# Kernel optimization log

Hardware: AMD Instinct MI355X
Metric: run time of the kernel (lower is better)

The kernel has to match this reference:

```python
import jax, jax.numpy as jnp
from jax import lax
import numpy as np

SIGMA = 25.0
NUM_STEPS = 100
DT = 0.01
SQRT_DT = float(np.sqrt(DT))


def _score(x, eig, t, cond, W1, we, wt, b1, Wc, W2, b2):
    # x: [B,S,H], eig: [B,S], t: scalar, cond: [B,S,H] or None
    h = x @ W1 + eig[..., None] * we + t * wt + b1
    if cond is not None:
        h = h + cond @ Wc
    h = jax.nn.silu(h)
    return h @ W2 + b2


def _diffuse(x_T, eigvals, eigvecs, cond, params, key):
    # reverse SDE from t=1 to t=0 in NUM_STEPS steps
    ts = jnp.linspace(1.0, 0.0, NUM_STEPS)
    keys = jax.random.split(key, NUM_STEPS)
    VT = jnp.swapaxes(eigvecs, -2, -1)  # [B,S,S]

    def step(x, tk):
        t, k = tk
        x_spec = VT @ x                                   # spectral projection [B,S,H]
        score = _score(x_spec, eigvals, t, cond, *params)
        drift = -(SIGMA ** (2.0 * t)) * score
        noise = jax.random.normal(k, x.shape, x.dtype)
        x_new = x - drift * DT + (SIGMA ** t) * SQRT_DT * noise
        return x_new, None

    x, _ = lax.scan(step, x_T, (ts, keys))
    return x


def _make_net(key, H, scale):
    k = jax.random.split(key, 4)
    return dict(
        W1=jax.random.normal(k[0], (H, H), jnp.float32) * scale,
        we=jax.random.normal(k[1], (H,), jnp.float32) * scale,
        wt=jax.random.normal(k[2], (H,), jnp.float32) * scale,
        b1=jnp.zeros((H,), jnp.float32),
        Wc=jax.random.normal(k[3], (H, H), jnp.float32) * scale,
        W2=jax.random.normal(jax.random.fold_in(key, 99), (H, H), jnp.float32) * scale,
        b2=jnp.zeros((H,), jnp.float32),
    )


def setup_inputs() -> dict:
    key = jax.random.key(0)
    B, S, H = 4, 512, 256
    ks = jax.random.split(key, 9)
    inp = {}
    inp['features_text'] = jax.random.normal(ks[0], (B, S, H), jnp.float32)
    inp['features_audio'] = jax.random.normal(ks[1], (B, S, H), jnp.float32)
    inp['features_visual'] = jax.random.normal(ks[2], (B, S, H), jnp.float32)
    sg = jax.random.normal(ks[3], (B, S, S), jnp.float32)
    inp['speaker_graph'] = 0.5 * (sg + jnp.swapaxes(sg, -2, -1))  # symmetric for eigh
    tg = jax.random.normal(ks[4], (B, S, S), jnp.float32)
    inp['temporal_graph'] = 0.5 * (tg + jnp.swapaxes(tg, -2, -1))
    # only text modality (index 0) is missing -> diffusion path for text only
    inp['missing_mask'] = jnp.zeros((B, S, 3), bool).at[:, :, 0].set(True)
    inp['x_T'] = jax.random.normal(ks[5], (B, S, H), jnp.float32)
    scale = 1.0 / np.sqrt(H)
    for prefix, k in [('ts', ks[6]), ('tt', ks[7])]:  # text_speaker / text_temporal nets
        net = _make_net(k, H, scale)
        for name, v in net.items():
            inp[f'{prefix}_{name}'] = v
    kr = jax.random.split(ks[8], 2)
    inp['rec_W'] = jax.random.normal(kr[0], (H, H), jnp.float32) * scale
    inp['rec_b'] = jnp.zeros((H,), jnp.float32)
    return inp


def reference(features_text, features_audio, features_visual,
              speaker_graph, temporal_graph, missing_mask, x_T,
              ts_W1, ts_we, ts_wt, ts_b1, ts_Wc, ts_W2, ts_b2,
              tt_W1, tt_we, tt_wt, tt_b1, tt_Wc, tt_W2, tt_b2,
              rec_W, rec_b):
    # spectral decomposition of both graphs
    s_vals, s_vecs = jnp.linalg.eigh(speaker_graph)
    t_vals, t_vecs = jnp.linalg.eigh(temporal_graph)

    feats = {'text': features_text, 'audio': features_audio, 'visual': features_visual}
    miss = np.asarray(missing_mask)  # concrete branching as in torch forward
    any_missing = [bool(miss[:, :, i].any()) for i in range(3)]

    params = {'text': (
        (ts_W1, ts_we, ts_wt, ts_b1, ts_Wc, ts_W2, ts_b2),
        (tt_W1, tt_we, tt_wt, tt_b1, tt_Wc, tt_W2, tt_b2))}
    key = jax.random.key(42)

    recovered = {}
    for i, modality in enumerate(['text', 'audio', 'visual']):
        if any_missing[i]:
            # condition = mean of present (non-missing) other modalities
            cond_feats = [feats[m] for j, m in enumerate(['text', 'audio', 'visual'])
                          if m != modality and not any_missing[j]]
            cond = None
            if cond_feats:
                cond = jnp.mean(jnp.stack(cond_feats, axis=-1), axis=-1)
            k_s, k_t = jax.random.split(jax.random.fold_in(key, i))
            p_s, p_t = params[modality]
            x_s = _diffuse(x_T, s_vals, s_vecs, cond, p_s, k_s)
            x_t = _diffuse(x_T, t_vals, t_vecs, cond, p_t, k_t)
            rec = 0.5 * (x_s + x_t)
            recovered[modality] = rec @ rec_W + rec_b
        else:
            recovered[modality] = feats[modality]
    return (recovered['text'], recovered['audio'], recovered['visual'])
```

## Files before the change

kernel.cpp:

```cpp
#include <hip/hip_runtime.h>
#include <math.h>
#include <stdint.h>


#define NT 256
#define SZF 131072
#define MATSZ 262144
#define NB 32
#define ILAST 384
#define TBASE (ILAST+1)
#define TSZ (512-TBASE)

#define BD_DK   0
#define BD_ZK   4096
#define BD_RZK  8192
#define BD_TAU  12288
#define BD_DS   16384
#define BD_RHO  20480
#define BD_KSK  20736
#define BD_KIDX 22784
#define BD_DIDX 24832
#define BD_PERM 26880
#define BD_CNT  28928

#define ALD(p)    __hip_atomic_load((p),  __ATOMIC_RELAXED, __HIP_MEMORY_SCOPE_AGENT)
#define AST(p,v)  __hip_atomic_store((p), (v), __ATOMIC_RELAXED, __HIP_MEMORY_SCOPE_AGENT)

__host__ __device__ static inline unsigned rotl32(unsigned v, int r){ return (v<<r)|(v>>(32-r)); }

__host__ __device__ static inline void tf2x32(unsigned k0, unsigned k1,
                                              unsigned x0, unsigned x1,
                                              unsigned* o0, unsigned* o1){
  unsigned ks2 = k0 ^ k1 ^ 0x1BD11BDAu;
  x0 += k0; x1 += k1;
#define TF4(r0,r1,r2,r3) \
  x0 += x1; x1 = rotl32(x1,r0); x1 ^= x0; \
  x0 += x1; x1 = rotl32(x1,r1); x1 ^= x0; \
  x0 += x1; x1 = rotl32(x1,r2); x1 ^= x0; \
  x0 += x1; x1 = rotl32(x1,r3); x1 ^= x0;
  TF4(13,15,26,6)  x0 += k1;  x1 += ks2 + 1u;
  TF4(17,29,16,24) x0 += ks2; x1 += k0 + 2u;
  TF4(13,15,26,6)  x0 += k0;  x1 += k1 + 3u;
  TF4(17,29,16,24) x0 += k1;  x1 += ks2 + 4u;
  TF4(13,15,26,6)  x0 += ks2; x1 += k0 + 5u;
#undef TF4
  *o0 = x0; *o1 = x1;
}

__device__ static inline float erfinv_xla(float x){
  float w = -log1pf(-x*x);
  float p;
  if (w < 5.0f){
    w -= 2.5f;
    p = 2.81022636e-08f;
    p = fmaf(p, w, 3.43273939e-07f);
    p = fmaf(p, w, -3.5233877e-06f);
    p = fmaf(p, w, -4.39150654e-06f);
    p = fmaf(p, w, 0.00021858087f);
    p = fmaf(p, w, -0.00125372503f);
    p = fmaf(p, w, -0.00417768164f);
    p = fmaf(p, w, 0.246640727f);
    p = fmaf(p, w, 1.50140941f);
  } else {
    w = sqrtf(w) - 3.0f;
    p = -0.000200214257f;
    p = fmaf(p, w, 0.000100950558f);
    p = fmaf(p, w, 0.00134934322f);
    p = fmaf(p, w, -0.00367342844f);
    p = fmaf(p, w, 0.00573950773f);
    p = fmaf(p, w, -0.0076224613f);
    p = fmaf(p, w, 0.00943887047f);
    p = fmaf(p, w, 1.00167406f);
    p = fmaf(p, w, 2.83297682f);
  }
  return p*x;
}

__device__ static inline float bits_to_normal(unsigned bits){
  const float MINV = -0.99999994f;
  float f = __uint_as_float((bits >> 9) | 0x3f800000u) - 1.0f;
  float u = fmaxf(MINV, fmaf(f, 2.0f, MINV));
  return 1.41421356237309515f * erfinv_xla(u);
}

__device__ __forceinline__ void gbar2(unsigned* slots, int sg, int g, unsigned epoch){
  __threadfence_block();
  __syncthreads();
  int t = threadIdx.x;
  if (t == 0) AST(slots + (sg*NB + g)*16, epoch);
  if (t < NB){
    unsigned* sl = slots + (sg*NB + t)*16;
    while (ALD(sl) < epoch){ __builtin_amdgcn_s_sleep(1); }
  }
  __syncthreads();
}

__global__ __launch_bounds__(256) void k_sytd2_lds(const float* Gs, const float* Gt,
                                                   double* Vb, double* smalls,
                                                   unsigned* slots, double* Atail){
  int sg = blockIdx.x / NB, g = blockIdx.x % NB;
  const float* G = (sg < 4) ? (Gs + (size_t)sg*MATSZ) : (Gt + (size_t)(sg-4)*MATSZ);
  double* V = Vb + (size_t)sg*MATSZ;
  double* d  = smalls + (size_t)sg*512;
  double* e  = smalls + 4096 + (size_t)sg*512;
  double* tu = smalls + 8192 + (size_t)sg*512;
  double* acc0 = smalls + 274688 + (size_t)sg*512;
  double* acc1 = acc0 + 4096;
  double* col0 = smalls + 282880 + (size_t)sg*512;
  double* col1 = col0 + 4096;
  double* vvh  = smalls + 291072 + (size_t)sg*512;
  double* At = Atail + (size_t)sg*MATSZ;
  int t = threadIdx.x, wave = t >> 6, lane = t & 63;

  __shared__ double Arows[16][512];
  __shared__ double vv[512], wv[512], col2[512], acc[512];
  __shared__ double red[4];
  __shared__ double bc[4];

  for (int j=0; j<16; j++){
    int r = 32*j + g;
    for (int c=t; c<512; c+=256)
      Arows[j][c] = (double)G[(size_t)r*512 + c];
  }

  for (int r=t; r<512; r+=256) col2[r] = (r>=1) ? (double)G[(size_t)r*512] : 0.0;
  __syncthreads();
  {
    double part = 0.0;
    for (int r=2+t; r<512; r+=256) part += col2[r]*col2[r];
    #pragma unroll
    for (int off=32; off; off>>=1) part += __shfl_down(part, off, 64);
    if (lane==0) red[wave]=part;
    __syncthreads();
    if (t==0){
      double xsq = red[0]+red[1]+red[2]+red[3];
      double alpha = col2[1];
      double beta,tv,scal;
      if (xsq == 0.0){ beta=alpha; tv=0.0; scal=0.0; }
      else {
        beta = -copysign(sqrt(alpha*alpha + xsq), alpha);
        tv = (beta - alpha)/beta;
        scal = 1.0/(alpha - beta);
      }
      if (g==0){ e[0]=beta; tu[0]=tv; }
      bc[0]=tv; bc[1]=scal;
    }
  }
  __syncthreads();
  double tauv = bc[0];
  {
    double scal = bc[1];
    for (int r=t; r<512; r+=256){
      double v = 0.0;
      if (r==1) v = 1.0;
      else if (r>1) v = (tauv==0.0) ? 0.0 : col2[r]*scal;
      vv[r]=v;
      if (r>=1 && (r & (NB-1))==g) V[r] = v;
    }
  }
  __syncthreads();
  if (g==0){
    for (int r=1+t; r<512; r+=256) AST(&col0[r], (double)G[(size_t)r*512 + 1]);
  }
  {
    int r0 = 1 + ((g - 1) & (NB-1));
    for (int r = r0 + NB*wave; r < 512; r += 4*NB){
      const double* Ar = Arows[r>>5];
      double p = 0.0;
      for (int c=lane; c<512; c+=64) p += Ar[c]*vv[c];
      #pragma unroll
      for (int off=32; off; off>>=1) p += __shfl_down(p, off, 64);
      if (lane==0) AST(&acc0[r], p);
    }
  }

  for (int i=0; i<ILAST; i++){
    gbar2(slots, sg, g, (unsigned)(i+1));
    int lo=i+1, lo2=i+2;
    double* accR = (i&1) ? acc1 : acc0;
    double* colR = (i&1) ? col1 : col0;
    double* accW = (i&1) ? acc0 : acc1;
    double* colW = (i&1) ? col0 : col1;
    double part = 0.0;
    for (int r=lo+t; r<512; r+=256){
      double a_ = ALD(&accR[r]);
      double c_ = ALD(&colR[r]);
      acc[r]=a_; col2[r]=c_;
      part += (tauv*a_)*vv[r];
    }
    #pragma unroll
    for (int off=32; off; off>>=1) part += __shfl_down(part, off, 64);
    if (lane==0) red[wave]=part;
    __syncthreads();
    {
      double dot = red[0]+red[1]+red[2]+red[3];
      double alpha2 = -0.5*tauv*dot;
      double vlo = vv[lo];
      double wlo = fma(alpha2, vlo, tauv*acc[lo]);
      for (int r=lo+t; r<512; r+=256){
        double wr = fma(alpha2, vv[r], tauv*acc[r]);
        wv[r]=wr;
        col2[r] = col2[r] - vv[r]*wlo - wr*vlo;
      }
    }
    __syncthreads();
    part = 0.0;
    for (int r=lo2+1+t; r<512; r+=256) part += col2[r]*col2[r];
    #pragma unroll
    for (int off=32; off; off>>=1) part += __shfl_down(part, off, 64);
    if (lane==0) red[wave]=part;
    __syncthreads();
    double tau2, scal2;
    {
      double xsq = red[0]+red[1]+red[2]+red[3];
      double alpha = col2[lo2];
      double beta;
      if (xsq == 0.0){ beta=alpha; tau2=0.0; scal2=0.0; }
      else {
        beta = -copysign(sqrt(alpha*alpha + xsq), alpha);
        tau2 = (beta - alpha)/beta;
        scal2 = 1.0/(alpha - beta);
      }
      if (t==0 && g==0){ e[lo]=beta; tu[lo]=tau2; }
    }
    {
      double vvc[8], wvc[8], v2c[8];
      #pragma unroll
      for (int j=0;j<8;j++){
        int c = lo + lane + 64*j;
        bool ok = c < 512;
        vvc[j] = ok ? vv[c] : 0.0;
        wvc[j] = ok ? wv[c] : 0.0;
        double v2v = 0.0;
        if (ok){
          if (c==lo2) v2v = 1.0;
          else if (c>lo2) v2v = (tau2==0.0) ? 0.0 : col2[c]*scal2;
        }
        v2c[j] = v2v;
      }
      int r0 = lo + ((g - lo) & (NB-1));
      for (int r = r0 + NB*wave; r < 512; r += 4*NB){
        double* Ar = Arows[r>>5];
        double vr = vv[r], wr = wv[r];
        double p = 0.0;
        #pragma unroll
        for (int j=0;j<8;j++){
          int c = lo + lane + 64*j;
          if (c < 512){
            double an = Ar[c] - vr*wvc[j] - wr*vvc[j];
            Ar[c] = an;
            p += an * v2c[j];
            if (c == lo2) AST(&colW[r], an);
          }
        }
        #pragma unroll
        for (int off=32; off; off>>=1) p += __shfl_down(p, off, 64);
        if (lane==0) AST(&accW[r], p);
      }
    }
    __syncthreads();
    for (int r=t; r<512; r+=256){
      double v = 0.0;
      if (r==lo2) v = 1.0;
      else if (r>lo2) v = (tau2==0.0) ? 0.0 : col2[r]*scal2;
      vv[r]=v;
      if (r>=lo2 && (r & (NB-1))==g) V[(size_t)lo*512 + r] = v;
    }
    tauv = tau2;
  }

  if (t < 16){
    int r = 32*t + g;
    if (r <= ILAST) d[r] = Arows[t][r];
  }
  for (int j=0; j<16; j++){
    int r = 32*j + g;
    if (r >= TBASE){
      for (int c=TBASE+t; c<512; c+=256)
        At[(size_t)r*512 + c] = Arows[j][c];
    }
  }
  if (g==0){
    for (int r=t; r<512; r+=256) vvh[r] = vv[r];
  }
}

__global__ __launch_bounds__(256) void k_sy_tail(const double* Atail, double* Vb,
                                                 double* smalls){
  int sg = blockIdx.x;
  double* V = Vb + (size_t)sg*MATSZ;
  double* d  = smalls + (size_t)sg*512;
  double* e  = smalls + 4096 + (size_t)sg*512;
  double* tu = smalls + 8192 + (size_t)sg*512;
  const double* accG = smalls + 274688 + (size_t)sg*512;
  const double* colG = smalls + 282880 + (size_t)sg*512;
  const double* vvG  = smalls + 291072 + (size_t)sg*512;
  const double* At0 = Atail + (size_t)sg*MATSZ;
  int t = threadIdx.x, wave = t >> 6, lane = t & 63;

  __shared__ double At[TSZ*128];
  __shared__ double vv[512], wv[512], col2[512], acc[512], accN[512], colN[512];
  __shared__ double red[4];

  for (int rl=0; rl<TSZ; rl++)
    for (int cl=t; cl<TSZ; cl+=256)
      At[rl*128+cl] = At0[(size_t)(TBASE+rl)*512 + TBASE+cl];
  for (int r=t; r<512; r+=256){
    if (r >= ILAST){ vv[r]=vvG[r]; acc[r]=accG[r]; col2[r]=colG[r]; }
  }
  double tauv = tu[ILAST];
  __syncthreads();

  for (int i=ILAST; i<510; i++){
    int lo=i+1, lo2=i+2;
    double part = 0.0;
    for (int r=lo+t; r<512; r+=256) part += (tauv*acc[r])*vv[r];
    #pragma unroll
    for (int off=32; off; off>>=1) part += __shfl_down(part, off, 64);
    if (lane==0) red[wave]=part;
    __syncthreads();
    {
      double dot = red[0]+red[1]+red[2]+red[3];
      double alpha2 = -0.5*tauv*dot;
      double vlo = vv[lo];
      double wlo = fma(alpha2, vlo, tauv*acc[lo]);
      for (int r=lo+t; r<512; r+=256){
        double wr = fma(alpha2, vv[r], tauv*acc[r]);
        wv[r]=wr;
        col2[r] = col2[r] - vv[r]*wlo - wr*vlo;
      }
    }
    __syncthreads();
    part = 0.0;
    for (int r=lo2+1+t; r<512; r+=256) part += col2[r]*col2[r];
    #pragma unroll
    for (int off=32; off; off>>=1) part += __shfl_down(part, off, 64);
    if (lane==0) red[wave]=part;
    __syncthreads();
    double tau2, scal2;
    {
      double xsq = red[0]+red[1]+red[2]+red[3];
      double alpha = col2[lo2];
      double beta;
      if (xsq == 0.0){ beta=alpha; tau2=0.0; scal2=0.0; }
      else {
        beta = -copysign(sqrt(alpha*alpha + xsq), alpha);
        tau2 = (beta - alpha)/beta;
        scal2 = 1.0/(alpha - beta);
      }
      if (t==0){ e[lo]=beta; tu[lo]=tau2; }
    }
    {
      double vvc[8], wvc[8], v2c[8];
      #pragma unroll
      for (int j=0;j<8;j++){
        int c = lo + lane + 64*j;
        bool ok = c < 512;
        vvc[j] = ok ? vv[c] : 0.0;
        wvc[j] = ok ? wv[c] : 0.0;
        double v2v = 0.0;
        if (ok){
          if (c==lo2) v2v = 1.0;
          else if (c>lo2) v2v = (tau2==0.0) ? 0.0 : col2[c]*scal2;
        }
        v2c[j] = v2v;
      }
      for (int r = lo + wave; r < 512; r += 4){
        double* Ar = &At[(r-TBASE)*128];
        double vr = vv[r], wr = wv[r];
        double p = 0.0;
        #pragma unroll
        for (int j=0;j<8;j++){
          int c = lo + lane + 64*j;
          if (c < 512){
            double an = Ar[c-TBASE] - vr*wvc[j] - wr*vvc[j];
            Ar[c-TBASE] = an;
            p += an * v2c[j];
            if (c == lo2) colN[r] = an;
          }
        }
        #pragma unroll
        for (int off=32; off; off>>=1) p += __shfl_down(p, off, 64);
        if (lane==0) accN[r] = p;
      }
    }
    __syncthreads();
    for (int r=t; r<512; r+=256){
      if (r >= lo2){
        double v = (r==lo2) ? 1.0 : ((tau2==0.0) ? 0.0 : col2[r]*scal2);
        vv[r]=v;
        V[(size_t)lo*512 + r] = v;
        col2[r] = colN[r];
        acc[r] = accN[r];
      }
    }
    tauv = tau2;
    __syncthreads();
  }
  for (int rl=t; rl<TSZ; rl+=256) d[TBASE+rl] = At[rl*128+rl];
}

__global__ void k_scale(double* smalls, int sbase){
  int sg = sbase + blockIdx.x, t = threadIdx.x;
  double* d = smalls + (size_t)sg*512;
  double* e = smalls + 4096 + (size_t)sg*512;
  __shared__ double red[256];
  double m = 0.0;
  for (int i=t;i<512;i+=256) m = fmax(m, fabs(d[i]));
  for (int i=t;i<511;i+=256) m = fmax(m, fabs(e[i]));
  red[t]=m; __syncthreads();
  for (int off=128; off; off>>=1){ if (t<off) red[t]=fmax(red[t],red[t+off]); __syncthreads(); }
  double org = red[0]; if (org == 0.0) org = 1.0;
  if (t==0) smalls[12288+sg] = org;
  double inv = 1.0/org;
  __syncthreads();
  for (int i=t;i<512;i+=256) d[i] *= inv;
  for (int i=t;i<511;i+=256) e[i] *= inv;
}

__global__ void k_tear(double* smalls, int sbase){
  int t = threadIdx.x;
  int sg = sbase + (t >> 5), k = (t & 31) + 1;
  if (k <= 31){
    double* d = smalls + (size_t)sg*512;
    double* e = smalls + 4096 + (size_t)sg*512;
    double ae = fabs(e[16*k - 1]);
    d[16*k - 1] -= ae;
    d[16*k]     -= ae;
  }
}

__global__ __launch_bounds__(256) void k_leaves(double* smalls, double* Zb, int sbase){
  __shared__ double LA[4][256];
  __shared__ double LQ[4][256];
  int t = threadIdx.x, w = t >> 6, lane = t & 63;
  int L = blockIdx.x*4 + w;
  int s_local = L >> 5;
  int sg = sbase + s_local;
  int leaf = L & 31;
  double* dd = smalls + (size_t)sg*512;
  double* ee = smalls + 4096 + (size_t)sg*512;
  double* Z = Zb + (size_t)s_local*MATSZ;
  int base = leaf*16;
  double* A = LA[w]; double* Q = LQ[w];

  for (int i=lane; i<256; i+=64){ A[i]=0.0; Q[i]=0.0; }
  __builtin_amdgcn_sched_barrier(0);
  if (lane < 16){ A[lane*17] = dd[base+lane]; Q[lane*17] = 1.0; }
  if (lane < 15){
    double ev = ee[base+lane];
    A[lane*16+lane+1] = ev; A[(lane+1)*16+lane] = ev;
  }
  __builtin_amdgcn_sched_barrier(0);
  double nr = 0.0;
  if (lane == 0){ for (int i=0;i<256;i++) nr += A[i]*A[i]; }
  nr = __shfl(nr, 0, 64);
  double thr = nr*1e-30 + 1e-300;

  for (int sweep=0; sweep<60; sweep++){
    double offs = 0.0;
    for (int p=0;p<15;p++) for (int q=p+1;q<16;q++){
      double apq = A[p*16+q];
      offs += 2.0*apq*apq;
      if (apq == 0.0) continue;
      double theta = 0.5*(A[q*17]-A[p*17])/apq;
      double tt;
      if (fabs(theta) > 1e18) tt = 0.5/theta;
      else tt = copysign(1.0, theta)/(fabs(theta)+sqrt(theta*theta+1.0));
      double cc = 1.0/sqrt(tt*tt+1.0), ss = tt*cc;
      __builtin_amdgcn_sched_barrier(0);
      if (lane < 16){
        int k = lane;
        double akp=A[k*16+p], akq=A[k*16+q];
        A[k*16+p] = cc*akp - ss*akq;
        A[k*16+q] = ss*akp + cc*akq;
      }
      __builtin_amdgcn_sched_barrier(0);
      if (lane < 16){
        int k = lane;
        double apk=A[p*16+k], aqk=A[q*16+k];
        A[p*16+k] = cc*apk - ss*aqk;
        A[q*16+k] = ss*apk + cc*aqk;
      }
      __builtin_amdgcn_sched_barrier(0);
      if (lane < 16){
        int k = lane;
        double qkp=Q[k*16+p], qkq=Q[k*16+q];
        Q[k*16+p] = cc*qkp - ss*qkq;
        Q[k*16+q] = ss*qkp + cc*qkq;
      }
      __builtin_amdgcn_sched_barrier(0);
    }
    if (offs < thr) break;
  }
  __builtin_amdgcn_sched_barrier(0);
  if (lane == 0){
    for (int i=0;i<16;i++){
      int mi=i;
      for (int j=i+1;j<16;j++) if (A[j*17] < A[mi*17]) mi=j;
      if (mi!=i){
        double tmp=A[i*17]; A[i*17]=A[mi*17]; A[mi*17]=tmp;
        for (int k=0;k<16;k++){ double q1=Q[k*16+i]; Q[k*16+i]=Q[k*16+mi]; Q[k*16+mi]=q1; }
      }
    }
  }
  __builtin_amdgcn_sched_barrier(0);
  if (lane < 16) dd[base+lane] = A[lane*17];
  for (int i=lane; i<256; i+=64){
    int r = i >> 4, c = i & 15;
    Z[(size_t)(base+r)*512 + base + c] = Q[i];
  }
}

__global__ __launch_bounds__(256) void k_deflate(double* smalls, const double* Zsrc_b,
                                                 double* bscr, int level, int sbase){
  const double EPS32 = 5.9604644775390625e-8;
  const double ISQ2  = 0.70710678118654752440;
  int s_local = blockIdx.x;
  int sg = sbase + s_local;
  int hh = 16 << level, n = hh << 1;
  int merge = blockIdx.y, start = merge*n;
  double* d = smalls + (size_t)sg*512;
  const double* e = smalls + 4096 + (size_t)sg*512;
  const double* Z = Zsrc_b + (size_t)s_local*MATSZ;
  double* rotg = smalls + 12544 + (size_t)(sg*32+merge)*1024;
  double* dkG  = bscr + BD_DK  + (size_t)s_local*512 + start;
  double* zkG  = bscr + BD_ZK  + (size_t)s_local*512 + start;
  double* rzkG = bscr + BD_RZK + (size_t)s_local*512 + start;
  double* dsG  = bscr + BD_DS  + (size_t)s_local*512 + start;
  double* rhoG = bscr + BD_RHO;
  int* kidxG = (int*)(bscr + BD_KIDX) + s_local*512 + start;
  int* didxG = (int*)(bscr + BD_DIDX) + s_local*512 + start;
  int* permG = (int*)(bscr + BD_PERM) + s_local*512 + start;
  int* cntG  = (int*)(bscr + BD_CNT) + (s_local*32+merge)*2;

  __shared__ double ds[512], zl[512];
  __shared__ double rc[256], rs[256];
  __shared__ double red[256];
  __shared__ double sv[2];
  __shared__ int perm[512], kidx[512], didx[512];
  __shared__ int rp[256], rq[256];
  __shared__ int counts[2];
  int t = threadIdx.x;
  if (t == 0){
    int i=0, j=hh, k=0;
    while (i < hh && j < n){
      if (d[start+i] <= d[start+j]) perm[k++]=i++; else perm[k++]=j++;
    }
    while (i < hh) perm[k++]=i++;
    while (j < n)  perm[k++]=j++;
  }
  __syncthreads();
  double eb = e[start+hh-1];
  double rho = 2.0*fabs(eb);
  double sgn = (eb < 0.0) ? -1.0 : 1.0;
  for (int i=t; i<n; i+=NT){
    int p = perm[i];
    ds[i] = d[start+p];
    double zr = (p < hh) ? Z[(size_t)(start+hh-1)*512 + start + p]
                         : sgn * Z[(size_t)(start+hh)*512 + start + p];
    zl[i] = zr * ISQ2;
  }
  __syncthreads();
  double m = 0.0;
  for (int i=t;i<n;i+=NT) m = fmax(m, fabs(zl[i]));
  red[t]=m; __syncthreads();
  for (int off=128; off; off>>=1){ if (t<off) red[t]=fmax(red[t],red[t+off]); __syncthreads(); }
  if (t==0) sv[0] = red[0];
  __syncthreads();
  m = 0.0;
  for (int i=t;i<n;i+=NT) m = fmax(m, fabs(ds[i]));
  red[t]=m; __syncthreads();
  for (int off=128; off; off>>=1){ if (t<off) red[t]=fmax(red[t],red[t+off]); __syncthreads(); }
  if (t==0) sv[1] = red[0];
  __syncthreads();
  double zmaxv = sv[0];
  double tol = 8.0*EPS32*fmax(sv[1], zmaxv);

  if (t == 0){
    int K=0, nd=0, nrot=0;
    if (rho*zmaxv <= tol){
      for (int j=0;j<n;j++) didx[nd++]=j;
    } else {
      int pj = -1;
      for (int j=0;j<n;j++){
        if (rho*fabs(zl[j]) <= tol){
          didx[nd++]=j;
        } else if (pj < 0){
          pj = j;
        } else {
          double s_ = zl[pj], c_ = zl[j];
          double tau2 = sqrt(c_*c_ + s_*s_);
          double tdf = ds[j] - ds[pj];
          double cc = c_/tau2, sr = -s_/tau2;
          if (fabs(tdf*cc*sr) <= tol){
            zl[j] = tau2; zl[pj] = 0.0;
            if (nrot < 256){
              rp[nrot]=perm[pj]; rq[nrot]=perm[j]; rc[nrot]=cc; rs[nrot]=sr; nrot++;
            }
            double tn = ds[pj]*cc*cc + ds[j]*sr*sr;
            ds[j]  = ds[pj]*sr*sr + ds[j]*cc*cc;
            ds[pj] = tn;
            didx[nd++] = pj;
            pj = j;
          } else {
            kidx[K++] = pj;
            pj = j;
          }
        }
      }
      if (pj >= 0) kidx[K++] = pj;
    }
    for (int a=1;a<nd;a++){
      int v = didx[a]; double dv = ds[v]; int b = a-1;
      while (b >= 0 && ds[didx[b]] > dv){ didx[b+1]=didx[b]; b--; }
      didx[b+1] = v;
    }
    counts[0]=K; counts[1]=nd;
    cntG[0]=K; cntG[1]=nd;
    rhoG[s_local*32+merge] = rho;
    rotg[0] = (double)nrot;
    for (int i=0;i<nrot;i++){
      rotg[1+4*i]=(double)rp[i]; rotg[2+4*i]=(double)rq[i];
      rotg[3+4*i]=rc[i]; rotg[4+4*i]=rs[i];
    }
  }
  __syncthreads();
  int K = counts[0], nd = counts[1];
  for (int k=t; k<K; k+=NT){
    int ki = kidx[k];
    double dv = ds[ki], zv = zl[ki];
    dkG[k]=dv; zkG[k]=zv; rzkG[k]=(rho*zv)*zv; kidxG[k]=ki;
  }
  for (int j=t; j<n;  j+=NT){ dsG[j]=ds[j]; permG[j]=perm[j]; }
  for (int j=t; j<nd; j+=NT) didxG[j]=didx[j];
}

__global__ __launch_bounds__(256) void k_bisect(double* bscr, int level, int split){
  int s_local = blockIdx.x;
  int hh = 16 << level, n = hh << 1;
  int merge = blockIdx.y, start = merge*n;
  const double* dkG  = bscr + BD_DK  + (size_t)s_local*512 + start;
  const double* zkG  = bscr + BD_ZK  + (size_t)s_local*512 + start;
  const double* rzkG = bscr + BD_RZK + (size_t)s_local*512 + start;
  double* taukG = bscr + BD_TAU + (size_t)s_local*512 + start;
  int* KskG = (int*)(bscr + BD_KSK) + s_local*512 + start;
  const int* cntG = (int*)(bscr + BD_CNT) + (s_local*32+merge)*2;
  double rho = (bscr + BD_RHO)[s_local*32+merge];
  __shared__ double dks[512], rzks[512], zks[512];
  int t = threadIdx.x;
  int K = cntG[0];
  for (int i=t;i<K;i+=NT){ dks[i]=dkG[i]; rzks[i]=rzkG[i]; zks[i]=zkG[i]; }
  __syncthreads();
  int lane = t & 63, w = t >> 6;
  for (int j2 = blockIdx.z*4 + w; j2 < K; j2 += split*4){
    int Kb; double lo, hi;
    if (j2 < K-1){
      double mid = 0.5*(dks[j2+1]-dks[j2]);
      double dj = dks[j2];
      double part = 0.0;
      for (int i=lane;i<K;i+=64){ double dif=(dks[i]-dj)-mid; part += rzks[i]/dif; }
      #pragma unroll
      for (int off=32; off; off>>=1) part += __shfl_xor(part, off, 64);
      double gg = 1.0 + part;
      if (gg >= 0.0){ Kb=j2;   lo=0.0;  hi=mid; }
      else          { Kb=j2+1; lo=-mid; hi=0.0; }
    } else {
      double part = 0.0;
      for (int i=lane;i<K;i+=64) part += zks[i]*zks[i];
      #pragma unroll
      for (int off=32; off; off>>=1) part += __shfl_xor(part, off, 64);
      Kb=K-1; lo=0.0; hi=rho*part + 1e-300;
    }
    double dK = dks[Kb];
    for (int it=0; it<72; it++){
      double mid = 0.5*(lo+hi);
      if (mid==lo || mid==hi) break;
      double part = 0.0;
      for (int i=lane;i<K;i+=64){ double dif=(dks[i]-dK)-mid; part += rzks[i]/dif; }
      #pragma unroll
      for (int off=32; off; off>>=1) part += __shfl_xor(part, off, 64);
      double gg = 1.0 + part;
      if (gg < 0.0) lo=mid; else hi=mid;
    }
    if (lane==0){ KskG[j2]=Kb; taukG[j2]=0.5*(lo+hi); }
  }
}

__global__ __launch_bounds__(256) void k_sfin(double* smalls, double* Sm_b,
                                              const double* bscr, int level, int sbase){
  int s_local = blockIdx.x;
  int sg = sbase + s_local;
  int hh = 16 << level, n = hh << 1;
  int merge = blockIdx.y, start = merge*n;
  double* d = smalls + (size_t)sg*512;
  double* Sm = Sm_b + (size_t)s_local*MATSZ;
  const double* dkG  = bscr + BD_DK  + (size_t)s_local*512 + start;
  const double* zkG  = bscr + BD_ZK  + (size_t)s_local*512 + start;
  const double* taukG= bscr + BD_TAU + (size_t)s_local*512 + start;
  const double* dsG  = bscr + BD_DS  + (size_t)s_local*512 + start;
  const int* KskG = (int*)(bscr + BD_KSK) + s_local*512 + start;
  const int* kidxG= (int*)(bscr + BD_KIDX) + s_local*512 + start;
  const int* didxG= (int*)(bscr + BD_DIDX) + s_local*512 + start;
  const int* permG= (int*)(bscr + BD_PERM) + s_local*512 + start;
  const int* cntG = (int*)(bscr + BD_CNT) + (s_local*32+merge)*2;
  double rho = (bscr + BD_RHO)[s_local*32+merge];
  __shared__ double dk[512], zk[512], tauk[512], zh[512], outlam[512], ds[512];
  __shared__ int Ksk[512], kidx[512], didx[512], perm[512], outid[512];
  int t = threadIdx.x;
  int K = cntG[0], nd = cntG[1];
  for (int i=t;i<K;i+=NT){
    dk[i]=dkG[i]; zk[i]=zkG[i]; tauk[i]=taukG[i]; Ksk[i]=KskG[i]; kidx[i]=kidxG[i];
  }
  for (int i=t;i<n;i+=NT){ ds[i]=dsG[i]; perm[i]=permG[i]; }
  for (int i=t;i<nd;i+=NT) didx[i]=didxG[i];
  __syncthreads();
  for (int i=t; i<K; i+=NT){
    double P = (Ksk[i]==i) ? tauk[i] : (dk[Ksk[i]]-dk[i]) + tauk[i];
    for (int j=0;j<K;j++){
      if (j==i) continue;
      double num = (dk[Ksk[j]]-dk[i]) + tauk[j];
      double den = dk[j]-dk[i];
      P *= num/den;
    }
    zh[i] = copysign(sqrt(fabs(P/rho)), zk[i]);
  }
  __syncthreads();
  if (t == 0){
    int a=0, b=0;
    for (int j=0;j<n;j++){
      double la = (a<K)  ? (dk[Ksk[a]]+tauk[a]) : 1e300;
      double lb = (b<nd) ? ds[didx[b]]          : 1e300;
      if (la <= lb){ outid[j]=a;     outlam[j]=la; a++; }
      else         { outid[j]=512+b; outlam[j]=lb; b++; }
    }
  }
  __syncthreads();
  for (int j=t; j<n; j+=NT) d[start+j] = outlam[j];
  for (int j=t; j<n; j+=NT){
    double* col = Sm + (size_t)(start+j)*512;
    int id = outid[j];
    for (int i=0;i<n;i++) col[i]=0.0;
    if (id >= 512){
      col[perm[didx[id-512]]] = 1.0;
    } else {
      int k = id;
      double ss_ = 0.0;
      for (int i=0;i<K;i++){
        double dif = (dk[i]-dk[Ksk[k]]) - tauk[k];
        if (dif == 0.0) dif = 1e-300;
        double v = zh[i]/dif;
        col[perm[kidx[i]]] = v; ss_ += v*v;
      }
      double inv = 1.0/sqrt(ss_);
      for (int i=0;i<K;i++) col[perm[kidx[i]]] *= inv;
    }
  }
}

__global__ __launch_bounds__(256) void k_rot(double* Sm_b, const double* smalls,
                                             int level, int sbase){
  int s_local = blockIdx.x, merge = blockIdx.y;
  int sg = sbase + s_local;
  int hh = 16 << level, n = hh << 1, start = merge*n;
  const double* rotg = smalls + 12544 + (size_t)(sg*32+merge)*1024;
  double* Sm = Sm_b + (size_t)s_local*MATSZ;
  int cnt = (int)rotg[0];
  for (int i=cnt-1; i>=0; i--){
    int p = (int)rotg[1+4*i], q = (int)rotg[2+4*i];
    double c = rotg[3+4*i], sr = rotg[4+4*i];
    for (int j=threadIdx.x; j<n; j+=256){
      double* col = Sm + (size_t)(start+j)*512;
      double a = col[p], b = col[q];
      col[p] = c*a - sr*b;
      col[q] = sr*a + c*b;
    }
    __syncthreads();
  }
}

__global__ __launch_bounds__(256) void k_gemm64(const double* Zsrc_b, const double* Sm_b,
                                                double* Zdst_b, int level){
  int hh = 16 << level, n = hh << 1;
  int mpm = 512 / n;
  int bz = blockIdx.z;
  int s = bz / mpm, merge = bz % mpm;
  int start = merge*n;
  const double* Zs = Zsrc_b + (size_t)s*MATSZ;
  const double* Sm = Sm_b + (size_t)s*MATSZ;
  double* Zd = Zdst_b + (size_t)s*MATSZ;
  int row0 = start + blockIdx.y*32, col0 = start + blockIdx.x*32;
  int t = threadIdx.x;
  int tr = t >> 4, tc = t & 15;
  __shared__ double As[32][33];
  __shared__ double Bs[32][33];
  double a00=0,a01=0,a10=0,a11=0;
  for (int q0=0; q0<n; q0+=32){
    #pragma unroll
    for (int it=0; it<4; it++){
      int idx = t + it*256;
      int r = idx >> 5, q = idx & 31;
      As[r][q] = Zs[(size_t)(row0+r)*512 + start + q0 + q];
    }
    #pragma unroll
    for (int it=0; it<4; it++){
      int idx = t + it*256;
      int c = idx >> 5, q = idx & 31;
      Bs[q][c] = Sm[(size_t)(col0+c)*512 + q0 + q];
    }
    __syncthreads();
    #pragma unroll 8
    for (int q=0;q<32;q++){
      double ar0=As[tr][q], ar1=As[tr+16][q];
      double bc0=Bs[q][tc], bc1=Bs[q][tc+16];
      a00 = fma(ar0,bc0,a00); a01 = fma(ar0,bc1,a01);
      a10 = fma(ar1,bc0,a10); a11 = fma(ar1,bc1,a11);
    }
    __syncthreads();
  }
  Zd[(size_t)(row0+tr)*512 + col0+tc]       = a00;
  Zd[(size_t)(row0+tr)*512 + col0+tc+16]    = a01;
  Zd[(size_t)(row0+tr+16)*512 + col0+tc]    = a10;
  Zd[(size_t)(row0+tr+16)*512 + col0+tc+16] = a11;
}

__global__ __launch_bounds__(256) void k_backq(double* Z2_b, const double* Vh_b,
                                               const double* smalls, int sbase){
  int s_local = blockIdx.x, cb = blockIdx.y;
  int sg = sbase + s_local;
  double* Z = Z2_b + (size_t)s_local*MATSZ;
  const double* V = Vh_b + (size_t)sg*MATSZ;
  const double* tu = smalls + 8192 + (size_t)sg*512;
  int cg = threadIdx.x >> 5, lane = threadIdx.x & 31;
  int c = cb*8 + cg;
  __shared__ double zc[8][512];
  for (int r=lane; r<512; r+=32) zc[cg][r] = Z[(size_t)r*512 + c];
  for (int i=509; i>=0; i--){
    double tv = tu[i];
    if (tv == 0.0) continue;
    double wp = 0.0;
    for (int r=i+1+lane; r<512; r+=32) wp += V[(size_t)i*512 + r]*zc[cg][r];
    #pragma unroll
    for (int off=16; off; off>>=1) wp += __shfl_down(wp, off, 32);
    double w = __shfl(wp, 0, 32);
    double tw = tv*w;
    for (int r=i+1+lane; r<512; r+=32) zc[cg][r] -= tw*V[(size_t)i*512 + r];
  }
  for (int r=lane; r<512; r+=32) Z[(size_t)r*512 + c] = zc[cg][r];
}

__global__ void k_finalize(const double* Z2_b, const double* smalls,
                           float* Vs32, float* Vt32, float* eig, int sbase){
  int s_local = blockIdx.x;
  int sg = sbase + s_local;
  const double* Z = Z2_b + (size_t)s_local*MATSZ;
  float* Vt_pass = (sg < 4) ? (Vs32 + (size_t)sg*MATSZ)
                            : (Vt32 + (size_t)(sg-4)*MATSZ);
  double org = smalls[12288+sg];
  int idx = blockIdx.y*256 + threadIdx.x;
  int r = idx >> 9, c = idx & 511;
  Vt_pass[(size_t)c*512 + r] = (float)Z[(size_t)r*512 + c];
  if (idx < 512)
    eig[(size_t)sg*512 + idx] = (float)(smalls[(size_t)sg*512 + idx]*org);
}

struct KArgs {
  const float* Vt;
  const float* Vt2;
  float *xspec, *hbuf, *x, *E;
  const float *W1s, *W1t, *W2s, *W2t;
  const float *b2s, *b2t, *wts, *wtt, *b1s, *b1t, *wes, *wet;
  const float *cond, *Wcs, *Wct;
  const float *eig;
  const float *rec, *recW, *recb;
  float* out;
  float t, a, bc;
  unsigned nk0, nk1, nk2, nk3;
  int mode, nmat, ntx;
};

__global__ __launch_bounds__(256) void k_gemm32(KArgs P){
  int t = threadIdx.x;
  int L = blockIdx.x;
  int mat = L % P.nmat;
  int tile = L / P.nmat;
  int n0 = (tile % P.ntx) << 5;
  int m0 = (tile / P.ntx) << 6;
  const float *A, *B; float *C;
  int lda, K, chain = 0;
  if (P.mode == 0){
    A = (mat < 4) ? (P.Vt + (size_t)mat*MATSZ) : (P.Vt2 + (size_t)(mat-4)*MATSZ);
    lda = 512; K = 512;
    B = P.x + (size_t)mat*SZF; C = P.xspec + (size_t)mat*SZF;
  } else if (P.mode == 1){
    chain = mat >> 2;
    A = P.xspec + (size_t)mat*SZF; lda = 256; K = 256;
    B = chain ? P.W1t : P.W1s; C = P.hbuf + (size_t)mat*SZF;
  } else if (P.mode == 2){
    chain = mat >> 2;
    A = P.hbuf + (size_t)mat*SZF; lda = 256; K = 256;
    B = chain ? P.W2t : P.W2s; C = P.x + (size_t)mat*SZF;
  } else if (P.mode == 3){
    chain = mat;
    A = P.cond; lda = 256; K = 256;
    B = chain ? P.Wct : P.Wcs; C = P.E + (size_t)chain*4*SZF;
  } else {
    A = P.rec; lda = 256; K = 256;
    B = P.recW; C = P.out;
  }
  __shared__ float As[2][16][68];
  __shared__ float Bs[2][16][36];
  float acc[4][2] = {{0}};
  const int ra = t >> 2, kk4 = (t & 3) << 2;
  const int kb = (t & 127) >> 3, c4 = (t & 7) << 2;
  const int tr4 = (t >> 4) << 2, tc2 = (t & 15) << 1;
  const float* Aptr = &A[(size_t)(m0 + ra)*lda + kk4];
  const float* Bptr = &B[(size_t)kb*256 + n0 + c4];
  {
    const float4 av = *(const float4*)Aptr;
    As[0][kk4+0][ra]=av.x; As[0][kk4+1][ra]=av.y; As[0][kk4+2][ra]=av.z; As[0][kk4+3][ra]=av.w;
    if (t < 128){
      const float4 bv = *(const float4*)Bptr;
      *(float4*)&Bs[0][kb][c4] = bv;
    }
  }
  int buf = 0;
  for (int k0=0; k0<K; k0+=16){
    __syncthreads();
    bool more = (k0+16) < K;
    float4 avN, bvN;
    if (more){
      avN = *(const float4*)(Aptr + k0 + 16);
      if (t < 128) bvN = *(const float4*)(Bptr + (size_t)(k0+16)*256);
    }
    {
      const float (*Asb)[68] = As[buf];
      const float (*Bsb)[36] = Bs[buf];
      #pragma unroll
      for (int kk=0; kk<16; kk++){
        const float4 a4 = *(const float4*)&Asb[kk][tr4];
        const float2 b2 = *(const float2*)&Bsb[kk][tc2];
        const float ar[4] = {a4.x, a4.y, a4.z, a4.w};
        #pragma unroll
        for (int q=0;q<4;q++){
          acc[q][0] = fmaf(ar[q], b2.x, acc[q][0]);
          acc[q][1] = fmaf(ar[q], b2.y, acc[q][1]);
        }
      }
    }
    if (more){
      int nb = buf^1;
      As[nb][kk4+0][ra]=avN.x; As[nb][kk4+1][ra]=avN.y; As[nb][kk4+2][ra]=avN.z; As[nb][kk4+3][ra]=avN.w;
      if (t < 128) *(float4*)&Bs[nb][kb][c4] = bvN;
      buf = nb;
    }
  }
  #pragma unroll
  for (int q=0;q<4;q++){
    int r = m0 + tr4 + q;
    size_t rowoff = (size_t)r*256 + n0 + tc2;
    float2 cv;
    if (P.mode == 2) cv = *(const float2*)&C[rowoff];
    float res[2];
    #pragma unroll
    for (int p=0;p<2;p++){
      int c = n0 + tc2 + p;
      size_t oi = (size_t)r*256 + c;
      float v = acc[q][p];
      if (P.mode == 1){
        v += P.E[(size_t)mat*SZF + oi] + P.t * ((chain ? P.wtt : P.wts)[c]);
        float sg = 1.0f/(1.0f + expf(-v));
        v = v * sg;
      } else if (P.mode == 2){
        float bias = (chain ? P.b2t : P.b2s)[c];
        unsigned j = ((unsigned)(mat & 3))*131072u + (unsigned)oi;
        unsigned kk0 = chain ? P.nk2 : P.nk0;
        unsigned kk1 = chain ? P.nk3 : P.nk1;
        unsigned y0, y1;
        tf2x32(kk0, kk1, 0u, j, &y0, &y1);
        float nz = bits_to_normal(y0 ^ y1);
        float cx = (p==0) ? cv.x : cv.y;
        v = cx + P.a*(v + bias) + P.bc*nz;
      } else if (P.mode == 3){
        int bb = r >> 9, s2 = r & 511;
        v += (chain ? P.b1t : P.b1s)[c]
           + P.eig[(size_t)(chain*4 + bb)*512 + s2] * ((chain ? P.wet : P.wes)[c]);
      } else if (P.mode == 4){
        v += P.recb[c];
      }
      res[p] = v;
    }
    *(float2*)&C[rowoff] = make_float2(res[0], res[1]);
  }
}

__global__ void k_cond(float* cond, const float* a, const float* v){
  size_t i = (size_t)blockIdx.x*256 + threadIdx.x;
  cond[i] = 0.5f*(a[i] + v[i]);
}

__global__ void k_xinit(float* x, const float* xT){
  size_t i = (size_t)blockIdx.x*256 + threadIdx.x;
  size_t b = i >> 17, off = i & 131071;
  x[i] = xT[((b & 3) << 17) + off];
}

__global__ void k_rec(float* rec, const float* x){
  size_t i = (size_t)blockIdx.x*256 + threadIdx.x;
  rec[i] = 0.5f*(x[i] + x[i + 524288]);
}

__global__ void k_copy(float* out, const float* a, const float* v){
  size_t i = (size_t)blockIdx.x*256 + threadIdx.x;
  out[524288 + i] = (i < 524288) ? a[i] : v[i - 524288];
}

extern "C" void kernel_launch(void* const* d_in, const int* in_sizes, int n_in,
                              void* d_out, int out_size, void* d_ws, size_t ws_size,
                              hipStream_t stream){
  const float* f_audio   = (const float*)d_in[1];
  const float* f_visual  = (const float*)d_in[2];
  const float* g_speaker = (const float*)d_in[3];
  const float* g_temporal= (const float*)d_in[4];
  const float* x_T       = (const float*)d_in[6];
  const float* tsW1=(const float*)d_in[7],  *tswe=(const float*)d_in[8],
             * tswt=(const float*)d_in[9],  *tsb1=(const float*)d_in[10],
             * tsWc=(const float*)d_in[11], *tsW2=(const float*)d_in[12],
             * tsb2=(const float*)d_in[13];
  const float* ttW1=(const float*)d_in[14], *ttwe=(const float*)d_in[15],
             * ttwt=(const float*)d_in[16], *ttb1=(const float*)d_in[17],
             * ttWc=(const float*)d_in[18], *ttW2=(const float*)d_in[19],
             * ttb2=(const float*)d_in[20];
  const float* recW=(const float*)d_in[21], *recb=(const float*)d_in[22];
  float* out = (float*)d_out;

  const size_t MB = 1ull << 20;
  if (ws_size < 43*MB) return;
  bool wide = ws_size >= 80*MB;

  char* ws = (char*)d_ws;
  double* Vh     = (double*)(ws + 0);
  double* Atail  = (double*)(ws + 16*MB);
  double* A64    = (double*)(ws + 16*MB);
  double* Zb     = wide ? (double*)(ws + 48*MB) : (double*)(ws + 24*MB);
  double* Sm     = wide ? (double*)(ws + 64*MB) : (double*)(ws + 32*MB);
  double* smalls = (double*)(ws + 40*MB);
  unsigned* slots = (unsigned*)(smalls + 295168);
  float* Vt32_s  = (float*)(ws + 0);
  float* Vt32_t  = (float*)(ws + 8*MB);
  float* eig32   = (float*)(ws + 42*MB + 512*1024);
  double* bscr   = (double*)(ws + 42*MB + 640*1024);
  float* cond  = (float*)(ws + 16*MB);
  float* E     = (float*)(ws + 18*MB);
  float* xall  = (float*)(ws + 22*MB);
  float* xspec = (float*)(ws + 26*MB);
  float* hbuf  = (float*)(ws + 30*MB);

  unsigned f0, f1;
  tf2x32(0u, 42u, 0u, 0u, &f0, &f1);
  unsigned s0,s1,t0,t1;
  tf2x32(f0, f1, 0u, 0u, &s0, &s1);
  tf2x32(f0, f1, 0u, 1u, &t0, &t1);
  unsigned skeys[100][2], tkeys[100][2];
  for (int k=0; k<100; k++){
    tf2x32(s0, s1, 0u, (unsigned)k, &skeys[k][0], &skeys[k][1]);
    tf2x32(t0, t1, 0u, (unsigned)k, &tkeys[k][0], &tkeys[k][1]);
  }

  hipMemsetAsync(slots, 0, 16384, stream);

  k_sytd2_lds<<<8*NB, 256, 0, stream>>>(g_speaker, g_temporal, Vh, smalls, slots, Atail);
  k_sy_tail<<<8, 256, 0, stream>>>(Atail, Vh, smalls);

  int npass = wide ? 1 : 2;
  int nmat  = wide ? 8 : 4;
  for (int pass=0; pass<npass; pass++){
    int sbase = wide ? 0 : 4*pass;
    k_scale<<<nmat, 256, 0, stream>>>(smalls, sbase);
    hipMemsetAsync(Zb, 0, (size_t)(wide?16:8)*MB, stream);
    hipMemsetAsync(A64, 0, (size_t)(wide?16:8)*MB, stream);
    k_tear<<<1, nmat*32, 0, stream>>>(smalls, sbase);
    k_leaves<<<nmat*8, 256, 0, stream>>>(smalls, Zb, sbase);
    for (int level=0; level<5; level++){
      int n = 32 << level, mpm = 512/n;
      double* src = (level & 1) ? A64 : Zb;
      double* dst = (level & 1) ? Zb  : A64;
      int split = 2 << level;
      k_deflate<<<dim3(nmat, mpm), 256, 0, stream>>>(smalls, src, bscr, level, sbase);
      k_bisect<<<dim3(nmat, mpm, split), 256, 0, stream>>>(bscr, level, split);
      k_sfin<<<dim3(nmat, mpm), 256, 0, stream>>>(smalls, Sm, bscr, level, sbase);
      k_rot<<<dim3(nmat, mpm), 256, 0, stream>>>(Sm, smalls, level, sbase);
      k_gemm64<<<dim3(n/32, n/32, nmat*mpm), 256, 0, stream>>>(src, Sm, dst, level);
    }
    k_backq<<<dim3(nmat, 64), 256, 0, stream>>>(A64, Vh, smalls, sbase);
    k_finalize<<<dim3(nmat, 1024), 256, 0, stream>>>(A64, smalls,
                                                     Vt32_s, Vt32_t, eig32, sbase);
  }

  k_cond<<<2048, 256, 0, stream>>>(cond, f_audio, f_visual);
  k_xinit<<<4096, 256, 0, stream>>>(xall, x_T);

  KArgs P;
  P.Vt = Vt32_s; P.Vt2 = Vt32_t;
  P.xspec = xspec; P.hbuf = hbuf; P.x = xall; P.E = E;
  P.W1s = tsW1; P.W1t = ttW1; P.W2s = tsW2; P.W2t = ttW2;
  P.b2s = tsb2; P.b2t = ttb2; P.wts = tswt; P.wtt = ttwt;
  P.b1s = tsb1; P.b1t = ttb1; P.wes = tswe; P.wet = ttwe;
  P.cond = cond; P.Wcs = tsWc; P.Wct = ttWc;
  P.eig = eig32; P.rec = xspec; P.recW = recW; P.recb = recb; P.out = out;
  P.t = 0.f; P.a = 0.f; P.bc = 0.f;
  P.nk0 = 0; P.nk1 = 0; P.nk2 = 0; P.nk3 = 0;
  P.ntx = 8;

  P.mode = 3; P.nmat = 2;
  k_gemm32<<<512, 256, 0, stream>>>(P);

  for (int k=0; k<100; k++){
    float tf = (float)(1.0 - (double)k/99.0);
    float av = (float)(pow(25.0, 2.0*(double)tf) * 0.01);
    float bcv = (float)(pow(25.0, (double)tf) * 0.1);
    P.nk0 = skeys[k][0]; P.nk1 = skeys[k][1];
    P.nk2 = tkeys[k][0]; P.nk3 = tkeys[k][1];
    P.nmat = 8;
    P.mode = 0;
    k_gemm32<<<512, 256, 0, stream>>>(P);
    P.mode = 1; P.t = tf;
    k_gemm32<<<512, 256, 0, stream>>>(P);
    P.mode = 2; P.a = av; P.bc = bcv;
    k_gemm32<<<512, 256, 0, stream>>>(P);
  }

  k_rec<<<2048, 256, 0, stream>>>(xspec, xall);
  P.mode = 4; P.nmat = 1; P.rec = xspec;
  k_gemm32<<<256, 256, 0, stream>>>(P);
  k_copy<<<4096, 256, 0, stream>>>(out, f_audio, f_visual);
}
```

Measured before the change: 14.02 ms.

## Halve tridiagonalization blocks, widen GEMM k-tile, and fuse small elementwise kernels

Reduces blocks per matrix in the cooperative Householder tridiagonalization from 32 to 16, so each block holds 32 rows in LDS and fewer blocks take part in each grid barrier. It also adds a spin-count timeout to the barrier, folds the tear step into k_scale, and doubles the GEMM k-tile to 32 so there are fewer syncthreads per step. The cond/xinit and rec/copy elementwise kernels are merged to cut launch count. Using 16 blocks per matrix halves parallelism in the row updates, and the larger LDS footprint (over 128KB of doubles) may not fit or may lower occupancy.

```diff
diff --git a/kernel.cpp b/kernel.cpp
--- a/kernel.cpp
+++ b/kernel.cpp
@@ -6,7 +6,7 @@
 #define NT 256
 #define SZF 131072
 #define MATSZ 262144
-#define NB 32
+#define NB 16
 #define ILAST 384
 #define TBASE (ILAST+1)
 #define TSZ (512-TBASE)
@@ -83,14 +83,19 @@
   return 1.41421356237309515f * erfinv_xla(u);
 }
 
-__device__ __forceinline__ void gbar2(unsigned* slots, int sg, int g, unsigned epoch){
+__device__ __forceinline__ void gbar2(unsigned* slots, int sg, int g, unsigned epoch,
+                                      int* sdead){
   __threadfence_block();
   __syncthreads();
   int t = threadIdx.x;
   if (t == 0) AST(slots + (sg*NB + g)*16, epoch);
-  if (t < NB){
+  if (t < NB && !*sdead){
     unsigned* sl = slots + (sg*NB + t)*16;
-    while (ALD(sl) < epoch){ __builtin_amdgcn_s_sleep(1); }
+    int spins = 0;
+    while (ALD(sl) < epoch){
+      __builtin_amdgcn_s_sleep(1);
+      if (++spins > (1<<24)){ *sdead = 1; break; }
+    }
   }
   __syncthreads();
 }
@@ -112,13 +117,16 @@
   double* At = Atail + (size_t)sg*MATSZ;
   int t = threadIdx.x, wave = t >> 6, lane = t & 63;
 
-  __shared__ double Arows[16][512];
+  __shared__ double Arows[32][512];
   __shared__ double vv[512], wv[512], col2[512], acc[512];
   __shared__ double red[4];
   __shared__ double bc[4];
-
-  for (int j=0; j<16; j++){
-    int r = 32*j + g;
+  __shared__ int sdead;
+
+  if (t == 0) sdead = 0;
+
+  for (int j=0; j<32; j++){
+    int r = NB*j + g;
     for (int c=t; c<512; c+=256)
       Arows[j][c] = (double)G[(size_t)r*512 + c];
   }
@@ -165,7 +173,7 @@
   {
     int r0 = 1 + ((g - 1) & (NB-1));
     for (int r = r0 + NB*wave; r < 512; r += 4*NB){
-      const double* Ar = Arows[r>>5];
+      const double* Ar = Arows[r>>4];
       double p = 0.0;
       for (int c=lane; c<512; c+=64) p += Ar[c]*vv[c];
       #pragma unroll
@@ -175,7 +183,7 @@
   }
 
   for (int i=0; i<ILAST; i++){
-    gbar2(slots, sg, g, (unsigned)(i+1));
+    gbar2(slots, sg, g, (unsigned)(i+1), &sdead);
     int lo=i+1, lo2=i+2;
     double* accR = (i&1) ? acc1 : acc0;
     double* colR = (i&1) ? col1 : col0;
@@ -240,7 +248,7 @@
       }
       int r0 = lo + ((g - lo) & (NB-1));
       for (int r = r0 + NB*wave; r < 512; r += 4*NB){
-        double* Ar = Arows[r>>5];
+        double* Ar = Arows[r>>4];
         double vr = vv[r], wr = wv[r];
         double p = 0.0;
         #pragma unroll
@@ -269,12 +277,12 @@
     tauv = tau2;
   }
 
-  if (t < 16){
-    int r = 32*t + g;
+  if (t < 32){
+    int r = NB*t + g;
     if (r <= ILAST) d[r] = Arows[t][r];
   }
-  for (int j=0; j<16; j++){
-    int r = 32*j + g;
+  for (int j=0; j<32; j++){
+    int r = NB*j + g;
     if (r >= TBASE){
       for (int c=TBASE+t; c<512; c+=256)
         At[(size_t)r*512 + c] = Arows[j][c];
@@ -416,14 +424,9 @@
   __syncthreads();
   for (int i=t;i<512;i+=256) d[i] *= inv;
   for (int i=t;i<511;i+=256) e[i] *= inv;
-}
-
-__global__ void k_tear(double* smalls, int sbase){
-  int t = threadIdx.x;
-  int sg = sbase + (t >> 5), k = (t & 31) + 1;
-  if (k <= 31){
-    double* d = smalls + (size_t)sg*512;
-    double* e = smalls + 4096 + (size_t)sg*512;
+  __syncthreads();
+  if (t < 31){
+    int k = t + 1;
     double ae = fabs(e[16*k - 1]);
     d[16*k - 1] -= ae;
     d[16*k]     -= ae;
@@ -908,8 +911,8 @@
     A = P.rec; lda = 256; K = 256;
     B = P.recW; C = P.out;
   }
-  __shared__ float As[2][16][68];
-  __shared__ float Bs[2][16][36];
+  __shared__ float As[2][32][68];
+  __shared__ float Bs[2][32][36];
   float acc[4][2] = {{0}};
   const int ra = t >> 2, kk4 = (t & 3) << 2;
   const int kb = (t & 127) >> 3, c4 = (t & 7) << 2;
@@ -917,27 +920,35 @@
   const float* Aptr = &A[(size_t)(m0 + ra)*lda + kk4];
   const float* Bptr = &B[(size_t)kb*256 + n0 + c4];
   {
-    const float4 av = *(const float4*)Aptr;
-    As[0][kk4+0][ra]=av.x; As[0][kk4+1][ra]=av.y; As[0][kk4+2][ra]=av.z; As[0][kk4+3][ra]=av.w;
+    const float4 av  = *(const float4*)Aptr;
+    const float4 av2 = *(const float4*)(Aptr + 16);
+    As[0][kk4+0][ra]=av.x;  As[0][kk4+1][ra]=av.y;  As[0][kk4+2][ra]=av.z;  As[0][kk4+3][ra]=av.w;
+    As[0][16+kk4+0][ra]=av2.x; As[0][16+kk4+1][ra]=av2.y; As[0][16+kk4+2][ra]=av2.z; As[0][16+kk4+3][ra]=av2.w;
     if (t < 128){
-      const float4 bv = *(const float4*)Bptr;
+      const float4 bv  = *(const float4*)Bptr;
+      const float4 bv2 = *(const float4*)(Bptr + (size_t)16*256);
       *(float4*)&Bs[0][kb][c4] = bv;
+      *(float4*)&Bs[0][kb+16][c4] = bv2;
     }
   }
   int buf = 0;
-  for (int k0=0; k0<K; k0+=16){
-    __syncthreads();
-    bool more = (k0+16) < K;
-    float4 avN, bvN;
+  for (int k0=0; k0<K; k0+=32){
+    __syncthreads();
+    bool more = (k0+32) < K;
+    float4 avN, avN2, bvN, bvN2;
     if (more){
-      avN = *(const float4*)(Aptr + k0 + 16);
-      if (t < 128) bvN = *(const float4*)(Bptr + (size_t)(k0+16)*256);
+      avN  = *(const float4*)(Aptr + k0 + 32);
+      avN2 = *(const float4*)(Aptr + k0 + 48);
+      if (t < 128){
+        bvN  = *(const float4*)(Bptr + (size_t)(k0+32)*256);
+        bvN2 = *(const float4*)(Bptr + (size_t)(k0+48)*256);
+      }
     }
     {
       const float (*Asb)[68] = As[buf];
       const float (*Bsb)[36] = Bs[buf];
       #pragma unroll
-      for (int kk=0; kk<16; kk++){
+      for (int kk=0; kk<32; kk++){
         const float4 a4 = *(const float4*)&Asb[kk][tr4];
         const float2 b2 = *(const float2*)&Bsb[kk][tc2];
         const float ar[4] = {a4.x, a4.y, a4.z, a4.w};
@@ -950,8 +961,12 @@
     }
     if (more){
       int nb = buf^1;
-      As[nb][kk4+0][ra]=avN.x; As[nb][kk4+1][ra]=avN.y; As[nb][kk4+2][ra]=avN.z; As[nb][kk4+3][ra]=avN.w;
-      if (t < 128) *(float4*)&Bs[nb][kb][c4] = bvN;
+      As[nb][kk4+0][ra]=avN.x;  As[nb][kk4+1][ra]=avN.y;  As[nb][kk4+2][ra]=avN.z;  As[nb][kk4+3][ra]=avN.w;
+      As[nb][16+kk4+0][ra]=avN2.x; As[nb][16+kk4+1][ra]=avN2.y; As[nb][16+kk4+2][ra]=avN2.z; As[nb][16+kk4+3][ra]=avN2.w;
+      if (t < 128){
+        *(float4*)&Bs[nb][kb][c4] = bvN;
+        *(float4*)&Bs[nb][kb+16][c4] = bvN2;
+      }
       buf = nb;
     }
   }
@@ -994,24 +1009,18 @@
   }
 }
 
-__global__ void k_cond(float* cond, const float* a, const float* v){
-  size_t i = (size_t)blockIdx.x*256 + threadIdx.x;
-  cond[i] = 0.5f*(a[i] + v[i]);
-}
-
-__global__ void k_xinit(float* x, const float* xT){
+__global__ void k_init(float* cond, float* x, const float* a, const float* v,
+                       const float* xT){
   size_t i = (size_t)blockIdx.x*256 + threadIdx.x;
   size_t b = i >> 17, off = i & 131071;
   x[i] = xT[((b & 3) << 17) + off];
-}
-
-__global__ void k_rec(float* rec, const float* x){
+  if (i < 524288) cond[i] = 0.5f*(a[i] + v[i]);
+}
+
+__global__ void k_recc(float* rec, const float* x, float* out,
+                       const float* a, const float* v){
   size_t i = (size_t)blockIdx.x*256 + threadIdx.x;
-  rec[i] = 0.5f*(x[i] + x[i + 524288]);
-}
-
-__global__ void k_copy(float* out, const float* a, const float* v){
-  size_t i = (size_t)blockIdx.x*256 + threadIdx.x;
+  if (i < 524288) rec[i] = 0.5f*(x[i] + x[i + 524288]);
   out[524288 + i] = (i < 524288) ? a[i] : v[i - 524288];
 }
 
@@ -1079,7 +1088,6 @@
     k_scale<<<nmat, 256, 0, stream>>>(smalls, sbase);
     hipMemsetAsync(Zb, 0, (size_t)(wide?16:8)*MB, stream);
     hipMemsetAsync(A64, 0, (size_t)(wide?16:8)*MB, stream);
-    k_tear<<<1, nmat*32, 0, stream>>>(smalls, sbase);
     k_leaves<<<nmat*8, 256, 0, stream>>>(smalls, Zb, sbase);
     for (int level=0; level<5; level++){
       int n = 32 << level, mpm = 512/n;
@@ -1097,8 +1105,7 @@
                                                      Vt32_s, Vt32_t, eig32, sbase);
   }
 
-  k_cond<<<2048, 256, 0, stream>>>(cond, f_audio, f_visual);
-  k_xinit<<<4096, 256, 0, stream>>>(xall, x_T);
+  k_init<<<4096, 256, 0, stream>>>(cond, xall, f_audio, f_visual, x_T);
 
   KArgs P;
   P.Vt = Vt32_s; P.Vt2 = Vt32_t;
@@ -1130,8 +1137,7 @@
     k_gemm32<<<512, 256, 0, stream>>>(P);
   }
 
-  k_rec<<<2048, 256, 0, stream>>>(xspec, xall);
-  P.mode = 4; P.nmat = 1; P.rec = xspec;
+  k_recc<<<4096, 256, 0, stream>>>(xspec, xall, out, f_audio, f_visual);
+  P.mode = 4; P.nmat = 1;
   k_gemm32<<<256, 256, 0, stream>>>(P);
-  k_copy<<<4096, 256, 0, stream>>>(out, f_audio, f_visual);
-}
+}
```

Measured after the change: 14.13 ms. About the same (+0.8%).
